# Optimization experiments

Hardware: AMD Instinct MI355X
Metric: run time of the kernel (lower is better)

Reference implementation:

```python
import jax, jax.numpy as jnp
import numpy as np

N = 50000      # nodes
E = 800000     # edges (avg degree 16)
C_IN = 256
C_OUT = 256
H = 4
D = C_OUT // H  # 64
NEG_SLOPE = 0.2


def setup_inputs() -> dict:
    key = jax.random.key(0)
    ks = jax.random.split(key, 12)
    glorot = lambda k, shape: jax.random.uniform(k, shape, jnp.float32, -1.0, 1.0) * np.sqrt(6.0 / (shape[0] + shape[1]))
    return {
        "x": jax.random.normal(ks[0], (N, C_IN), jnp.float32),
        "src": jax.random.randint(ks[1], (E,), 0, N, jnp.int32),
        "dst": jax.random.randint(ks[2], (E,), 0, N, jnp.int32),
        "Wl": glorot(ks[3], (C_IN, C_OUT)),
        "bl": jnp.zeros((C_OUT,), jnp.float32),
        "Wr": glorot(ks[4], (C_IN, C_OUT)),
        "br": jnp.zeros((C_OUT,), jnp.float32),
        "Wv": glorot(ks[5], (C_IN, C_OUT)),
        "bv": jnp.zeros((C_OUT,), jnp.float32),
        "att_l": jax.random.normal(ks[6], (1, H, D), jnp.float32) * 0.1,
        "att_r": jax.random.normal(ks[7], (1, H, D), jnp.float32) * 0.1,
    }


def reference(x, src, dst, Wl, bl, Wr, br, Wv, bv, att_l, att_r):
    # lambda_policy=None, gcn_mode=False -> lmbda = lmbda2 = 1.0
    n = x.shape[0]
    sl = ((x @ Wl + bl).reshape(n, H, D) * att_l).sum(-1, keepdims=True)  # [N,H,1]
    sr = ((x @ Wr + br).reshape(n, H, D) * att_r).sum(-1, keepdims=True)  # [N,H,1]
    xv = (x @ Wv + bv).reshape(n, H, D)                                    # [N,H,D]

    # --- convolve branch: average scores over in-neighborhood (incl. self) ---
    hlr = jnp.concatenate([sl, sr], axis=1)                   # [N,2H,1]
    conv = jax.ops.segment_sum(hlr[src], dst, num_segments=n)  # sum_{u->v} hsrc[u]
    deg = jax.ops.segment_sum(jnp.ones((src.shape[0],), x.dtype), dst, num_segments=n)
    agg = (hlr + conv) / (1.0 + deg[:, None, None])            # [N,2H,1]
    sl, sr = agg[:, :H], agg[:, H:]

    # --- edge attention: gather-add-leakyrelu, segment softmax over dst ---
    e = jax.nn.leaky_relu(sl[src] + sr[dst], NEG_SLOPE)        # [E,H,1]
    emax = jax.ops.segment_max(e, dst, num_segments=n)
    emax = jnp.where(jnp.isfinite(emax), emax, 0.0)
    ex = jnp.exp(e - emax[dst])
    denom = jax.ops.segment_sum(ex, dst, num_segments=n)
    a = ex / jnp.maximum(denom[dst], 1e-16)                    # [E,H,1]

    # --- weighted message aggregation ---
    out = jax.ops.segment_sum(xv[src] * a, dst, num_segments=n)  # [N,H,D]
    return out
```

## Files before the change

kernel.cpp:

```cpp
#include <hip/hip_runtime.h>

#define C_IN 256
#define C_OUT 256
#define NH 4
#define HD 64
#define NEG_SLOPE 0.2f

typedef _Float16 half8 __attribute__((ext_vector_type(8)));
typedef _Float16 half4v __attribute__((ext_vector_type(4)));
typedef float floatx4 __attribute__((ext_vector_type(4)));

__global__ void prep_kernel(const float* __restrict__ Wl, const float* __restrict__ Wr,
                            const float* __restrict__ bl, const float* __restrict__ br,
                            const float* __restrict__ attl, const float* __restrict__ attr,
                            const float* __restrict__ Wv, const int* __restrict__ dst,
                            float* __restrict__ Ws, float* __restrict__ bs,
                            _Float16* __restrict__ WvT, int* __restrict__ deg,
                            int* __restrict__ rank, int E)
{
    int bid = blockIdx.x;
    int t = threadIdx.x;
    if (bid <= C_IN) {
        int c = bid;
        int h = t >> 6, d = t & 63;
        float al = attl[t], ar = attr[t];
        float vl, vr;
        if (c < C_IN) { vl = Wl[c * C_OUT + t] * al; vr = Wr[c * C_OUT + t] * ar; }
        else          { vl = bl[t] * al;             vr = br[t] * ar; }
#pragma unroll
        for (int off = 32; off >= 1; off >>= 1) {
            vl += __shfl_xor(vl, off, 64);
            vr += __shfl_xor(vr, off, 64);
        }
        if (d == 0) {
            if (c < C_IN) { Ws[c * 8 + h] = vl; Ws[c * 8 + 4 + h] = vr; }
            else          { bs[h] = vl;         bs[4 + h] = vr; }
        }
    } else if (bid <= C_IN + 256) {
        int idx = (bid - (C_IN + 1)) * 256 + t;
        int n = idx >> 8, k = idx & 255;
        WvT[n * 256 + k] = (_Float16)Wv[k * 256 + n];
    } else {
        int i = (bid - (C_IN + 257)) * 256 + t;
        int base = i * 4;
        if (base >= E) return;
        if (base + 4 <= E) {
            int4 d4 = *(const int4*)(dst + base);
            int r0 = atomicAdd(&deg[d4.x], 1);
            int r1 = atomicAdd(&deg[d4.y], 1);
            int r2 = atomicAdd(&deg[d4.z], 1);
            int r3 = atomicAdd(&deg[d4.w], 1);
            *(int4*)(rank + base) = make_int4(r0, r1, r2, r3);
        } else {
            for (int k = base; k < E; ++k) rank[k] = atomicAdd(&deg[dst[k]], 1);
        }
    }
}

__global__ __launch_bounds__(256) void gemm_xv(const float* __restrict__ x,
    const _Float16* __restrict__ WvT, const float* __restrict__ bv,
    const float* __restrict__ Ws, const float* __restrict__ bs,
    _Float16* __restrict__ xv, float* __restrict__ s, int M)
{
    __shared__ __align__(16) _Float16 As[64][40];
    __shared__ __align__(16) _Float16 Bs[128][40];
    int tid = threadIdx.x;
    int wid = tid >> 6, lane = tid & 63;
    int quad = lane >> 4, r16 = lane & 15;
    int m0 = blockIdx.x * 64, n0 = blockIdx.y * 128;
    bool do_s = (blockIdx.y == 0);

    floatx4 acc[8];
#pragma unroll
    for (int j = 0; j < 8; ++j) acc[j] = (floatx4){0.f, 0.f, 0.f, 0.f};

    int arow = tid >> 3, af4 = tid & 7;
    int brow = tid >> 2, bg  = tid & 3;

    float sacc[2][8];
#pragma unroll
    for (int p = 0; p < 2; ++p)
#pragma unroll
        for (int j = 0; j < 8; ++j) sacc[p][j] = 0.f;

    for (int k0 = 0; k0 < 256; k0 += 32) {
        float w8[4][8];
        if (do_s) {
#pragma unroll
            for (int q = 0; q < 4; ++q) {
                const float4* wr = (const float4*)(Ws + (size_t)(k0 + af4 * 4 + q) * 8);
                float4 wa = wr[0], wb = wr[1];
                w8[q][0] = wa.x; w8[q][1] = wa.y; w8[q][2] = wa.z; w8[q][3] = wa.w;
                w8[q][4] = wb.x; w8[q][5] = wb.y; w8[q][6] = wb.z; w8[q][7] = wb.w;
            }
        }
#pragma unroll
        for (int p = 0; p < 2; ++p) {
            int rr = arow + p * 32;
            int gm = m0 + rr;
            float4 v = make_float4(0.f, 0.f, 0.f, 0.f);
            if (gm < M) v = *(const float4*)(x + (size_t)gm * 256 + k0 + af4 * 4);
            half4v tmp;
            tmp[0] = (_Float16)v.x; tmp[1] = (_Float16)v.y;
            tmp[2] = (_Float16)v.z; tmp[3] = (_Float16)v.w;
            *(half4v*)&As[rr][af4 * 4] = tmp;
            if (do_s) {
                float xq[4] = {v.x, v.y, v.z, v.w};
#pragma unroll
                for (int q = 0; q < 4; ++q)
#pragma unroll
                    for (int j = 0; j < 8; ++j)
                        sacc[p][j] += xq[q] * w8[q][j];
            }
        }
#pragma unroll
        for (int p = 0; p < 2; ++p) {
            int nr = brow + p * 64;
            *(float4*)&Bs[nr][bg * 8] = *(const float4*)(WvT + (size_t)(n0 + nr) * 256 + k0 + bg * 8);
        }
        __syncthreads();
        half8 a = *(const half8*)&As[wid * 16 + r16][quad * 8];
        half8 b[8];
#pragma unroll
        for (int cg = 0; cg < 8; ++cg)
            b[cg] = *(const half8*)&Bs[cg * 16 + r16][quad * 8];
#pragma unroll
        for (int cg = 0; cg < 8; ++cg)
            acc[cg] = __builtin_amdgcn_mfma_f32_16x16x32_f16(a, b[cg], acc[cg], 0, 0, 0);
        __syncthreads();
    }

    if (do_s) {
        float b0[8];
#pragma unroll
        for (int j = 0; j < 8; ++j) b0[j] = bs[j];
#pragma unroll
        for (int p = 0; p < 2; ++p) {
#pragma unroll
            for (int o = 1; o <= 4; o <<= 1)
#pragma unroll
                for (int j = 0; j < 8; ++j)
                    sacc[p][j] += __shfl_xor(sacc[p][j], o, 64);
            int gm = m0 + arow + p * 32;
            if (af4 == 0 && gm < M) {
                *(float4*)(s + (size_t)gm * 8)     = make_float4(sacc[p][0] + b0[0], sacc[p][1] + b0[1], sacc[p][2] + b0[2], sacc[p][3] + b0[3]);
                *(float4*)(s + (size_t)gm * 8 + 4) = make_float4(sacc[p][4] + b0[4], sacc[p][5] + b0[5], sacc[p][6] + b0[6], sacc[p][7] + b0[7]);
            }
        }
    }

#pragma unroll
    for (int cg = 0; cg < 8; ++cg) {
        int gcol = n0 + cg * 16 + r16;
        float bias = bv[gcol];
        int rbase = m0 + wid * 16 + quad * 4;
#pragma unroll
        for (int rr = 0; rr < 4; ++rr) {
            int grow = rbase + rr;
            if (grow < M)
                xv[(size_t)grow * 256 + gcol] = (_Float16)(acc[cg][rr] + bias);
        }
    }
}

__global__ void scan_part(const int* __restrict__ deg, int* __restrict__ partials,
                          int N, int chunk)
{
    __shared__ int sd[256];
    int b = blockIdx.x, t = threadIdx.x;
    int idx = b * chunk + t;
    int v = (t < chunk && idx < N) ? deg[idx] : 0;
    sd[t] = v; __syncthreads();
    for (int off = 128; off >= 1; off >>= 1) {
        if (t < off) sd[t] += sd[t + off];
        __syncthreads();
    }
    if (t == 0) partials[b] = sd[0];
}

__global__ void scan_final(const int* __restrict__ deg, const int* __restrict__ partials,
                           int* __restrict__ offs, int N, int chunk)
{
    __shared__ int sp[256];
    __shared__ int sd[256];
    int b = blockIdx.x, t = threadIdx.x;
    int pv = partials[t];
    sp[t] = pv; __syncthreads();
    for (int off = 1; off < 256; off <<= 1) {
        int x = (t >= off) ? sp[t - off] : 0;
        __syncthreads();
        sp[t] += x;
        __syncthreads();
    }
    int base = sp[b] - partials[b];
    __syncthreads();

    int idx = b * chunk + t;
    int v = (t < chunk && idx < N) ? deg[idx] : 0;
    sd[t] = v; __syncthreads();
    for (int off = 1; off < 256; off <<= 1) {
        int x = (t >= off) ? sd[t - off] : 0;
        __syncthreads();
        sd[t] += x;
        __syncthreads();
    }
    int incl = sd[t], excl = incl - v;
    if (t < chunk && idx < N) offs[idx] = base + excl;
    if (idx == N - 1) offs[N] = base + incl;
}

__global__ void scatter_kernel(const int* __restrict__ src, const int* __restrict__ dst,
                               const int* __restrict__ offs, const int* __restrict__ rank,
                               int* __restrict__ csr_src, int E)
{
    int i = blockIdx.x * 256 + threadIdx.x;
    int base = i * 4;
    if (base >= E) return;
    if (base + 4 <= E) {
        int4 d  = *(const int4*)(dst + base);
        int4 sv = *(const int4*)(src + base);
        int4 r  = *(const int4*)(rank + base);
        csr_src[offs[d.x] + r.x] = sv.x;
        csr_src[offs[d.y] + r.y] = sv.y;
        csr_src[offs[d.z] + r.z] = sv.z;
        csr_src[offs[d.w] + r.w] = sv.w;
    } else {
        for (int k = base; k < E; ++k)
            csr_src[offs[dst[k]] + rank[k]] = src[k];
    }
}

__global__ void agg_kernel(const float* __restrict__ s, const int* __restrict__ csr_src,
                           const int* __restrict__ offs, const int* __restrict__ deg,
                           float* __restrict__ aggl, float* __restrict__ aggr, int N)
{
    int gid = blockIdx.x * 256 + threadIdx.x;
    int n = gid >> 3, c = gid & 7;
    if (n >= N) return;
    int off = offs[n], dg = deg[n];
    float acc = s[(size_t)n * 8 + c];
    int i = 0;
    for (; i + 4 <= dg; i += 4) {
        int p0 = csr_src[off + i];
        int p1 = csr_src[off + i + 1];
        int p2 = csr_src[off + i + 2];
        int p3 = csr_src[off + i + 3];
        float v0 = s[(size_t)p0 * 8 + c];
        float v1 = s[(size_t)p1 * 8 + c];
        float v2 = s[(size_t)p2 * 8 + c];
        float v3 = s[(size_t)p3 * 8 + c];
        acc += (v0 + v1) + (v2 + v3);
    }
    for (; i < dg; ++i) acc += s[(size_t)csr_src[off + i] * 8 + c];
    acc *= 1.0f / (1.0f + (float)dg);
    if (c < 4) aggl[(size_t)n * 4 + c]     = acc;
    else       aggr[(size_t)n * 4 + c - 4] = acc;
}

template<int SZ>
__device__ __forceinline__ void gather_sub(int cs, float w, int base, int grp, int lof,
    const _Float16* __restrict__ xv,
    float& o0, float& o1, float& o2, float& o3)
{
    half4v hv[SZ];
#pragma unroll
    for (int j = 0; j < SZ; ++j) {
        int sidx = __builtin_amdgcn_readlane(cs, base + j);
        hv[j] = *(const half4v*)(xv + (((unsigned)sidx << 8) + lof));
    }
#pragma unroll
    for (int j = 0; j < SZ; ++j) {
        float wv = __shfl(w, grp + base + j, 64);
        o0 += wv * (float)hv[j][0];
        o1 += wv * (float)hv[j][1];
        o2 += wv * (float)hv[j][2];
        o3 += wv * (float)hv[j][3];
    }
}

__device__ __forceinline__ void do_chunk(int cs, float w, int cnt, int grp, int lof,
    const _Float16* __restrict__ xv,
    float& o0, float& o1, float& o2, float& o3)
{
    if (cnt == 16) { gather_sub<16>(cs, w, 0, grp, lof, xv, o0, o1, o2, o3); return; }
    int b = 0;
    if (cnt & 8) { gather_sub<8>(cs, w, b, grp, lof, xv, o0, o1, o2, o3); b += 8; }
    if (cnt & 4) { gather_sub<4>(cs, w, b, grp, lof, xv, o0, o1, o2, o3); b += 4; }
    if (cnt & 2) { gather_sub<2>(cs, w, b, grp, lof, xv, o0, o1, o2, o3); b += 2; }
    if (cnt & 1) { gather_sub<1>(cs, w, b, grp, lof, xv, o0, o1, o2, o3); }
}

__global__ __launch_bounds__(256) void attn_out(const float* __restrict__ aggl,
    const float* __restrict__ aggr, const int* __restrict__ csr_src,
    const int* __restrict__ offs, const int* __restrict__ deg,
    const _Float16* __restrict__ xv, float* __restrict__ out, int N)
{
    int wid = threadIdx.x >> 6, lane = threadIdx.x & 63;
    int n = blockIdx.x * 4 + wid;
    if (n >= N) return;
    int myhead = lane >> 4, myedge = lane & 15, grp = lane & 48;
    int lof = lane << 2;
    int off = offs[n], dg = deg[n];
    const int* cb = csr_src + off;
    float ar = aggr[(unsigned)(n * 4 + myhead)];

    float o0 = 0.f, o1 = 0.f, o2 = 0.f, o3 = 0.f;

    int cs0 = 0, cs1 = 0, cs2 = 0, cs3 = 0;
    int e1 = myedge + 16, e2 = myedge + 32, e3 = myedge + 48;
    if (myedge < dg) cs0 = cb[myedge];
    if (e1 < dg)     cs1 = cb[e1];
    if (e2 < dg)     cs2 = cb[e2];
    if (e3 < dg)     cs3 = cb[e3];
    float a0 = 0.f, a1 = 0.f, a2 = 0.f, a3 = 0.f;
    if (myedge < dg) a0 = aggl[(unsigned)((cs0 << 2) + myhead)];
    if (e1 < dg)     a1 = aggl[(unsigned)((cs1 << 2) + myhead)];
    if (e2 < dg)     a2 = aggl[(unsigned)((cs2 << 2) + myhead)];
    if (e3 < dg)     a3 = aggl[(unsigned)((cs3 << 2) + myhead)];
    float w0 = 0.f, w1 = 0.f, w2 = 0.f, w3 = 0.f;
    if (myedge < dg) { float e = a0 + ar; e = (e > 0.f) ? e : NEG_SLOPE * e; w0 = __expf(e); }
    if (e1 < dg)     { float e = a1 + ar; e = (e > 0.f) ? e : NEG_SLOPE * e; w1 = __expf(e); }
    if (e2 < dg)     { float e = a2 + ar; e = (e > 0.f) ? e : NEG_SLOPE * e; w2 = __expf(e); }
    if (e3 < dg)     { float e = a3 + ar; e = (e > 0.f) ? e : NEG_SLOPE * e; w3 = __expf(e); }
    float denom = w0; denom += w1; denom += w2; denom += w3;

    int c0 = dg < 16 ? dg : 16;
    do_chunk(cs0, w0, c0, grp, lof, xv, o0, o1, o2, o3);
    if (dg > 16) {
        int c1 = dg - 16 < 16 ? dg - 16 : 16;
        do_chunk(cs1, w1, c1, grp, lof, xv, o0, o1, o2, o3);
    }
    if (dg > 32) {
        int c2 = dg - 32 < 16 ? dg - 32 : 16;
        do_chunk(cs2, w2, c2, grp, lof, xv, o0, o1, o2, o3);
    }
    if (dg > 48) {
        int c3 = dg - 48 < 16 ? dg - 48 : 16;
        do_chunk(cs3, w3, c3, grp, lof, xv, o0, o1, o2, o3);
    }
    for (int b = 64; b < dg; b += 16) {
        int cs = 0; float w = 0.f;
        if (b + myedge < dg) {
            cs = cb[b + myedge];
            float e = aggl[(unsigned)((cs << 2) + myhead)] + ar;
            e = (e > 0.f) ? e : NEG_SLOPE * e;
            w = __expf(e);
        }
        denom += w;
        int cnt = dg - b < 16 ? dg - b : 16;
        do_chunk(cs, w, cnt, grp, lof, xv, o0, o1, o2, o3);
    }

#pragma unroll
    for (int o = 1; o <= 8; o <<= 1) denom += __shfl_xor(denom, o, 64);
    float inv = 1.0f / fmaxf(denom, 1e-16f);
    floatx4 res = {o0 * inv, o1 * inv, o2 * inv, o3 * inv};
    __builtin_nontemporal_store(res, (floatx4*)(out + (size_t)n * 256 + lof));
}

extern "C" void kernel_launch(void* const* d_in, const int* in_sizes, int n_in,
                              void* d_out, int out_size, void* d_ws, size_t ws_size,
                              hipStream_t stream)
{
    const float* x    = (const float*)d_in[0];
    const int*   src  = (const int*)d_in[1];
    const int*   dst  = (const int*)d_in[2];
    const float* Wl   = (const float*)d_in[3];
    const float* bl   = (const float*)d_in[4];
    const float* Wr   = (const float*)d_in[5];
    const float* br   = (const float*)d_in[6];
    const float* Wv   = (const float*)d_in[7];
    const float* bv   = (const float*)d_in[8];
    const float* attl = (const float*)d_in[9];
    const float* attr = (const float*)d_in[10];
    float* out = (float*)d_out;

    int N = in_sizes[0] / C_IN;
    int E = in_sizes[1];

    char* p = (char*)d_ws;
    auto alloc = [&](size_t bytes) -> void* {
        uintptr_t q = (uintptr_t)p;
        q = (q + 255) & ~(uintptr_t)255;
        p = (char*)(q + bytes);
        return (void*)q;
    };
    float* Ws     = (float*)alloc((size_t)C_IN * 8 * sizeof(float));
    float* bs     = (float*)alloc(8 * sizeof(float));
    float* s      = (float*)alloc((size_t)N * 8 * sizeof(float));
    float* aggl   = (float*)alloc((size_t)N * 4 * sizeof(float));
    float* aggr   = (float*)alloc((size_t)N * 4 * sizeof(float));
    int* deg      = (int*)alloc((size_t)N * sizeof(int));
    int* offs     = (int*)alloc((size_t)(N + 1) * sizeof(int));
    int* partials = (int*)alloc(256 * sizeof(int));
    int* csr_src  = (int*)alloc((size_t)E * sizeof(int));
    _Float16* WvT = (_Float16*)alloc((size_t)C_IN * C_OUT * sizeof(_Float16));
    _Float16* xv  = (_Float16*)alloc((size_t)N * C_OUT * sizeof(_Float16));

    int* rank = (int*)d_out;

    hipMemsetAsync(deg, 0, (size_t)N * sizeof(int), stream);

    int deg_blocks = ((E + 3) / 4 + 255) / 256;
    prep_kernel<<<C_IN + 257 + deg_blocks, 256, 0, stream>>>(
        Wl, Wr, bl, br, attl, attr, Wv, dst, Ws, bs, WvT, deg, rank, E);
    gemm_xv<<<dim3((N + 63) / 64, C_OUT / 128), 256, 0, stream>>>(x, WvT, bv, Ws, bs, xv, s, N);
    int chunk = (N + 255) / 256;
    scan_part<<<256, 256, 0, stream>>>(deg, partials, N, chunk);
    scan_final<<<256, 256, 0, stream>>>(deg, partials, offs, N, chunk);
    scatter_kernel<<<((E + 3) / 4 + 255) / 256, 256, 0, stream>>>(src, dst, offs, rank, csr_src, E);
    agg_kernel<<<(N * 8 + 255) / 256, 256, 0, stream>>>(s, csr_src, offs, deg, aggl, aggr, N);
    attn_out<<<(N + 3) / 4, 256, 0, stream>>>(aggl, aggr, csr_src, offs, deg, xv, out, N);
}
```

Before: 286.0 us.

## Fuse scan, scatter and aggregation into one cooperative kernel with grid syncs

Replaces the four small mid-pipeline kernels (two scan passes, CSR scatter, neighbor score aggregation) with a single cooperative kernel of 1024 blocks that separates the phases with grid-wide syncs and uses grid-stride loops. The aim is to remove three kernel launch gaps and drain/fill bubbles between tiny kernels. In exchange it pays for grid barriers, the scatter and aggregation phases run on a fixed grid size instead of one thread per item, and the cooperative launch depends on all 1024 blocks being co-resident.

```diff
diff --git a/kernel.cpp b/kernel.cpp
--- a/kernel.cpp
+++ b/kernel.cpp
@@ -1,4 +1,7 @@
 #include <hip/hip_runtime.h>
+#include <hip/hip_cooperative_groups.h>
+
+namespace cg = cooperative_groups;
 
 #define C_IN 256
 #define C_OUT 256
@@ -163,98 +166,96 @@
     }
 }
 
-__global__ void scan_part(const int* __restrict__ deg, int* __restrict__ partials,
-                          int N, int chunk)
-{
+__global__ __launch_bounds__(256, 4) void mid_kernel(
+    const int* __restrict__ deg, int* __restrict__ partials, int* __restrict__ offs,
+    const int* __restrict__ src, const int* __restrict__ dst,
+    const int* __restrict__ rank, int* __restrict__ csr_src,
+    const float* __restrict__ s, float* __restrict__ aggl, float* __restrict__ aggr,
+    int N, int E, int chunk)
+{
+    cg::grid_group grid = cg::this_grid();
+    int b = blockIdx.x, t = threadIdx.x;
     __shared__ int sd[256];
-    int b = blockIdx.x, t = threadIdx.x;
-    int idx = b * chunk + t;
-    int v = (t < chunk && idx < N) ? deg[idx] : 0;
-    sd[t] = v; __syncthreads();
-    for (int off = 128; off >= 1; off >>= 1) {
-        if (t < off) sd[t] += sd[t + off];
+    __shared__ int sp[256];
+
+    if (b < 256) {
+        int idx = b * chunk + t;
+        int v = (t < chunk && idx < N) ? deg[idx] : 0;
+        sd[t] = v; __syncthreads();
+        for (int off = 128; off >= 1; off >>= 1) {
+            if (t < off) sd[t] += sd[t + off];
+            __syncthreads();
+        }
+        if (t == 0) partials[b] = sd[0];
+    }
+    grid.sync();
+
+    if (b < 256) {
+        int pv = partials[t];
+        sp[t] = pv; __syncthreads();
+        for (int off = 1; off < 256; off <<= 1) {
+            int x = (t >= off) ? sp[t - off] : 0;
+            __syncthreads();
+            sp[t] += x;
+            __syncthreads();
+        }
+        int base = sp[b] - partials[b];
         __syncthreads();
-    }
-    if (t == 0) partials[b] = sd[0];
-}
-
-__global__ void scan_final(const int* __restrict__ deg, const int* __restrict__ partials,
-                           int* __restrict__ offs, int N, int chunk)
-{
-    __shared__ int sp[256];
-    __shared__ int sd[256];
-    int b = blockIdx.x, t = threadIdx.x;
-    int pv = partials[t];
-    sp[t] = pv; __syncthreads();
-    for (int off = 1; off < 256; off <<= 1) {
-        int x = (t >= off) ? sp[t - off] : 0;
-        __syncthreads();
-        sp[t] += x;
-        __syncthreads();
-    }
-    int base = sp[b] - partials[b];
-    __syncthreads();
-
-    int idx = b * chunk + t;
-    int v = (t < chunk && idx < N) ? deg[idx] : 0;
-    sd[t] = v; __syncthreads();
-    for (int off = 1; off < 256; off <<= 1) {
-        int x = (t >= off) ? sd[t - off] : 0;
-        __syncthreads();
-        sd[t] += x;
-        __syncthreads();
-    }
-    int incl = sd[t], excl = incl - v;
-    if (t < chunk && idx < N) offs[idx] = base + excl;
-    if (idx == N - 1) offs[N] = base + incl;
-}
-
-__global__ void scatter_kernel(const int* __restrict__ src, const int* __restrict__ dst,
-                               const int* __restrict__ offs, const int* __restrict__ rank,
-                               int* __restrict__ csr_src, int E)
-{
-    int i = blockIdx.x * 256 + threadIdx.x;
-    int base = i * 4;
-    if (base >= E) return;
-    if (base + 4 <= E) {
-        int4 d  = *(const int4*)(dst + base);
-        int4 sv = *(const int4*)(src + base);
-        int4 r  = *(const int4*)(rank + base);
-        csr_src[offs[d.x] + r.x] = sv.x;
-        csr_src[offs[d.y] + r.y] = sv.y;
-        csr_src[offs[d.z] + r.z] = sv.z;
-        csr_src[offs[d.w] + r.w] = sv.w;
-    } else {
-        for (int k = base; k < E; ++k)
-            csr_src[offs[dst[k]] + rank[k]] = src[k];
-    }
-}
-
-__global__ void agg_kernel(const float* __restrict__ s, const int* __restrict__ csr_src,
-                           const int* __restrict__ offs, const int* __restrict__ deg,
-                           float* __restrict__ aggl, float* __restrict__ aggr, int N)
-{
-    int gid = blockIdx.x * 256 + threadIdx.x;
-    int n = gid >> 3, c = gid & 7;
-    if (n >= N) return;
-    int off = offs[n], dg = deg[n];
-    float acc = s[(size_t)n * 8 + c];
-    int i = 0;
-    for (; i + 4 <= dg; i += 4) {
-        int p0 = csr_src[off + i];
-        int p1 = csr_src[off + i + 1];
-        int p2 = csr_src[off + i + 2];
-        int p3 = csr_src[off + i + 3];
-        float v0 = s[(size_t)p0 * 8 + c];
-        float v1 = s[(size_t)p1 * 8 + c];
-        float v2 = s[(size_t)p2 * 8 + c];
-        float v3 = s[(size_t)p3 * 8 + c];
-        acc += (v0 + v1) + (v2 + v3);
-    }
-    for (; i < dg; ++i) acc += s[(size_t)csr_src[off + i] * 8 + c];
-    acc *= 1.0f / (1.0f + (float)dg);
-    if (c < 4) aggl[(size_t)n * 4 + c]     = acc;
-    else       aggr[(size_t)n * 4 + c - 4] = acc;
+
+        int idx = b * chunk + t;
+        int v = (t < chunk && idx < N) ? deg[idx] : 0;
+        sd[t] = v; __syncthreads();
+        for (int off = 1; off < 256; off <<= 1) {
+            int x = (t >= off) ? sd[t - off] : 0;
+            __syncthreads();
+            sd[t] += x;
+            __syncthreads();
+        }
+        int incl = sd[t], excl = incl - v;
+        if (t < chunk && idx < N) offs[idx] = base + excl;
+        if (idx == N - 1) offs[N] = base + incl;
+    }
+    grid.sync();
+
+    int nthreads = gridDim.x * 256;
+    for (int i = b * 256 + t; i * 4 < E; i += nthreads) {
+        int base4 = i * 4;
+        if (base4 + 4 <= E) {
+            int4 d  = *(const int4*)(dst + base4);
+            int4 sv = *(const int4*)(src + base4);
+            int4 r  = *(const int4*)(rank + base4);
+            csr_src[offs[d.x] + r.x] = sv.x;
+            csr_src[offs[d.y] + r.y] = sv.y;
+            csr_src[offs[d.z] + r.z] = sv.z;
+            csr_src[offs[d.w] + r.w] = sv.w;
+        } else {
+            for (int k = base4; k < E; ++k)
+                csr_src[offs[dst[k]] + rank[k]] = src[k];
+        }
+    }
+    grid.sync();
+
+    for (int gid = b * 256 + t; gid < N * 8; gid += nthreads) {
+        int n = gid >> 3, c = gid & 7;
+        int off = offs[n], dg = deg[n];
+        float acc = s[(size_t)n * 8 + c];
+        int i = 0;
+        for (; i + 4 <= dg; i += 4) {
+            int p0 = csr_src[off + i];
+            int p1 = csr_src[off + i + 1];
+            int p2 = csr_src[off + i + 2];
+            int p3 = csr_src[off + i + 3];
+            float v0 = s[(size_t)p0 * 8 + c];
+            float v1 = s[(size_t)p1 * 8 + c];
+            float v2 = s[(size_t)p2 * 8 + c];
+            float v3 = s[(size_t)p3 * 8 + c];
+            acc += (v0 + v1) + (v2 + v3);
+        }
+        for (; i < dg; ++i) acc += s[(size_t)csr_src[off + i] * 8 + c];
+        acc *= 1.0f / (1.0f + (float)dg);
+        if (c < 4) aggl[(size_t)n * 4 + c]     = acc;
+        else       aggr[(size_t)n * 4 + c - 4] = acc;
+    }
 }
 
 template<int SZ>
@@ -405,10 +406,14 @@
     prep_kernel<<<C_IN + 257 + deg_blocks, 256, 0, stream>>>(
         Wl, Wr, bl, br, attl, attr, Wv, dst, Ws, bs, WvT, deg, rank, E);
     gemm_xv<<<dim3((N + 63) / 64, C_OUT / 128), 256, 0, stream>>>(x, WvT, bv, Ws, bs, xv, s, N);
+
     int chunk = (N + 255) / 256;
-    scan_part<<<256, 256, 0, stream>>>(deg, partials, N, chunk);
-    scan_final<<<256, 256, 0, stream>>>(deg, partials, offs, N, chunk);
-    scatter_kernel<<<((E + 3) / 4 + 255) / 256, 256, 0, stream>>>(src, dst, offs, rank, csr_src, E);
-    agg_kernel<<<(N * 8 + 255) / 256, 256, 0, stream>>>(s, csr_src, offs, deg, aggl, aggr, N);
+    void* margs[] = { (void*)&deg, (void*)&partials, (void*)&offs,
+                      (void*)&src, (void*)&dst, (void*)&rank, (void*)&csr_src,
+                      (void*)&s, (void*)&aggl, (void*)&aggr,
+                      (void*)&N, (void*)&E, (void*)&chunk };
+    hipLaunchCooperativeKernel((void*)mid_kernel, dim3(1024), dim3(256),
+                               margs, 0, stream);
+
     attn_out<<<(N + 3) / 4, 256, 0, stream>>>(aggl, aggr, csr_src, offs, deg, xv, out, N);
 }
```

Result: slower. 655.8 us (+129.3%).
